# Kernel tuning notes

Measured on AMD Instinct MI355X. Metric: run time of the kernel, lower is better.

Reference implementation:

```python
import jax, jax.numpy as jnp
import numpy as np

B, N, D, H = 4, 2048, 64, 8

def setup_inputs() -> dict:
    key = jax.random.key(0)
    ks = jax.random.split(key, 6)
    s = 0.05
    return {
        "x":  jax.random.normal(ks[0], (B, N, D), dtype=jnp.float32),
        "Wq": jax.random.normal(ks[1], (D, D * H), dtype=jnp.float32) * s,
        "Wk": jax.random.normal(ks[2], (D, D * H), dtype=jnp.float32) * s,
        "Wv": jax.random.normal(ks[3], (D, D * H), dtype=jnp.float32) * s,
        "Wu": jax.random.normal(ks[4], (D * H, D), dtype=jnp.float32) * s,
        "bu": jnp.zeros((D,), dtype=jnp.float32),
    }

def reference(x, Wq, Wk, Wv, Wu, bu):
    b, n, d = x.shape
    h = Wq.shape[1] // d
    # projections: each head has full width d (per the original module)
    q = (x @ Wq).reshape(b, n, h, d).transpose(0, 2, 1, 3)  # [b,h,n,d]
    k = (x @ Wk).reshape(b, n, h, d).transpose(0, 2, 1, 3)
    v = (x @ Wv).reshape(b, n, h, d).transpose(0, 2, 1, 3)
    scores = jnp.einsum('bhnd,bhmd->bhnm', q, k) / jnp.sqrt(jnp.float32(d))
    w = jax.nn.softmax(scores, axis=-1)
    y = jnp.einsum('bhnm,bhmd->bhnd', w, v)          # [b,h,n,d]
    y = y.transpose(0, 2, 1, 3).reshape(b, n, h * d)  # [b,n,h*d]
    return y @ Wu + bu
```

## Files before the change

kernel.cpp:

```cpp
#include <hip/hip_runtime.h>
#include <hip/hip_bf16.h>

#define BB 4
#define NN 2048
#define DD 64
#define HH 8
#define DHH 512

typedef __bf16 bf16_t;
typedef __bf16 bf16x8 __attribute__((ext_vector_type(8)));
typedef __bf16 bf16x4 __attribute__((ext_vector_type(4)));
typedef float f32x4 __attribute__((ext_vector_type(4)));
typedef long long i64;
typedef i64 i64x2 __attribute__((ext_vector_type(2)));
typedef _Float16 f16_t;
typedef _Float16 f16x4 __attribute__((ext_vector_type(4)));
typedef __fp16 h16x2 __attribute__((ext_vector_type(2)));

__device__ __forceinline__ void dma16(const void* g, void* l) {
    __builtin_amdgcn_global_load_lds(
        (const __attribute__((address_space(1))) unsigned int*)g,
        (__attribute__((address_space(3))) unsigned int*)l,
        16, 0, 0);
}

#define MFMA   __builtin_amdgcn_mfma_f32_16x16x32_bf16
#define MFMA8  __builtin_amdgcn_mfma_f32_16x16x32_fp8_fp8
#define MFMA16F __builtin_amdgcn_mfma_f32_16x16x16f16

#define QSCALE 0.18033688011112042f


__global__ __launch_bounds__(256) void prep(
    const float* __restrict__ Wq, const float* __restrict__ Wk,
    const float* __restrict__ Wv, const float* __restrict__ Wu,
    bf16_t* __restrict__ Wqt, bf16_t* __restrict__ Wkt,
    bf16_t* __restrict__ Wvt, bf16_t* __restrict__ Wut)
{
    const int bid = blockIdx.x, tid = threadIdx.x;
    if (bid < 12) {
        const int m = bid >> 2, slice = bid & 3;
        const float* src = (m == 0) ? Wq : (m == 1) ? Wk : Wv;
        bf16_t* dst = (m == 0) ? Wqt : (m == 1) ? Wkt : Wvt;
        const float scale = (m == 0) ? QSCALE : 1.0f;
        const int dc = slice * 128 + (tid >> 1);
        const int kbase = (tid & 1) * 32;
        #pragma unroll
        for (int k0 = 0; k0 < 4; ++k0) {
            bf16x8 p;
            #pragma unroll
            for (int j = 0; j < 8; ++j)
                p[j] = (bf16_t)(src[(size_t)(kbase + k0 * 8 + j) * 512 + dc] * scale);
            *(bf16x8*)(dst + dc * 64 + kbase + k0 * 8) = p;
        }
    } else {
        const int kq = (bid - 12) * 128;
        const int dc = tid >> 2, sub = (tid & 3) * 32;
        #pragma unroll
        for (int k0 = 0; k0 < 4; ++k0) {
            bf16x8 p;
            #pragma unroll
            for (int j = 0; j < 8; ++j)
                p[j] = (bf16_t)Wu[(size_t)(kq + sub + k0 * 8 + j) * 64 + dc];
            *(bf16x8*)(Wut + dc * 512 + kq + sub + k0 * 8) = p;
        }
    }
}

__global__ __launch_bounds__(256) void qkv_mfma(
    const float* __restrict__ x, const bf16_t* __restrict__ Wqt,
    const bf16_t* __restrict__ Wkt, const bf16_t* __restrict__ Wvt,
    char* __restrict__ q8, char* __restrict__ k8, f16_t* __restrict__ vt)
{
    const int n0   = blockIdx.x * 64;
    const int h    = blockIdx.y;
    const int tid  = threadIdx.x;
    const int w    = tid >> 6;
    const int lane = tid & 63;
    const int quad = lane >> 4;
    const int c    = lane & 15;
    const int cq   = c & 7;
    const int l8   = lane >> 3;
    const int lg   = (lane & 7) ^ l8;
    const int lo   = l8 * 128 + lg * 16;
    const int sw0  = ((quad    ) ^ cq) * 16;
    const int sw1  = ((quad + 4) ^ cq) * 16;
    const int w2048 = w * 2048;

    __shared__ __align__(16) float  xs[64 * 64];
    __shared__ __align__(16) bf16_t Wqs[64 * 64], Wks[64 * 64], Wvs[64 * 64];

    {
        const int rloc = lane >> 4;
        const int s    = lane & 15;
        #pragma unroll
        for (int j = 0; j < 4; ++j) {
            int chunk = w * 4 + j;
            int r7 = (chunk * 4 + rloc) & 7;
            const char* src = (const char*)(x + (size_t)(n0 + chunk * 4 + rloc) * 64)
                            + ((s & 8) | ((s & 7) ^ r7)) * 16;
            dma16(src, (char*)xs + chunk * 1024);
        }
    }
    const char* qg = (const char*)Wqt + (size_t)h * 8192;
    const char* kg = (const char*)Wkt + (size_t)h * 8192;
    const char* vg = (const char*)Wvt + (size_t)h * 8192;
    dma16(qg + w2048 + lo,        (char*)Wqs + w2048);
    dma16(qg + w2048 + 1024 + lo, (char*)Wqs + w2048 + 1024);
    dma16(kg + w2048 + lo,        (char*)Wks + w2048);
    dma16(kg + w2048 + 1024 + lo, (char*)Wks + w2048 + 1024);
    dma16(vg + w2048 + lo,        (char*)Wvs + w2048);
    dma16(vg + w2048 + 1024 + lo, (char*)Wvs + w2048 + 1024);
    __syncthreads();

    auto xfrag = [&](int row, int kk) -> bf16x8 {
        const char* rbase = (const char*)xs + row * 256;
        int g0 = kk * 8 + ((quad * 2    ) ^ cq);
        int g1 = kk * 8 + ((quad * 2 + 1) ^ cq);
        f32x4 a = *(const f32x4*)(rbase + g0 * 16);
        f32x4 b = *(const f32x4*)(rbase + g1 * 16);
        bf16x8 r;
        r[0] = (bf16_t)a[0]; r[1] = (bf16_t)a[1]; r[2] = (bf16_t)a[2]; r[3] = (bf16_t)a[3];
        r[4] = (bf16_t)b[0]; r[5] = (bf16_t)b[1]; r[6] = (bf16_t)b[2]; r[7] = (bf16_t)b[3];
        return r;
    };

    bf16x8 xf0 = xfrag(w * 16 + c, 0);
    bf16x8 xf1 = xfrag(w * 16 + c, 1);

    const int gr = n0 + w * 16 + c;
    const int bb = gr >> 11, nn = gr & 2047;
    char* qrow_g = q8 + (((size_t)bb * HH + h) * NN + nn) * 64;
    char* krow_g = k8 + (((size_t)bb * HH + h) * NN + nn) * 64;
    const int nsw = nn & 3;

    #pragma unroll
    for (int mb = 0; mb < 4; ++mb) {
        const char* aq = (const char*)Wqs + (mb * 16 + c) * 128;
        const char* ak = (const char*)Wks + (mb * 16 + c) * 128;
        f32x4 accq = (f32x4){0.f, 0.f, 0.f, 0.f};
        f32x4 acck = (f32x4){0.f, 0.f, 0.f, 0.f};
        accq = MFMA(*(const bf16x8*)(aq + sw0), xf0, accq, 0, 0, 0);
        accq = MFMA(*(const bf16x8*)(aq + sw1), xf1, accq, 0, 0, 0);
        acck = MFMA(*(const bf16x8*)(ak + sw0), xf0, acck, 0, 0, 0);
        acck = MFMA(*(const bf16x8*)(ak + sw1), xf1, acck, 0, 0, 0);
        int g2  = (mb * 2 + (quad >> 1)) & 3;
        int off = ((quad & 1) * 4) + ((mb >> 1) * 8) + ((g2 ^ nsw) * 16);
        int pq = __builtin_amdgcn_cvt_pk_fp8_f32(accq[0], accq[1], 0, false);
        pq     = __builtin_amdgcn_cvt_pk_fp8_f32(accq[2], accq[3], pq, true);
        int pk = __builtin_amdgcn_cvt_pk_fp8_f32(acck[0], acck[1], 0, false);
        pk     = __builtin_amdgcn_cvt_pk_fp8_f32(acck[2], acck[3], pk, true);
        *(int*)(qrow_g + off) = pq;
        *(int*)(krow_g + off) = pk;
    }

    const char* wvrow = (const char*)Wvs + (w * 16 + c) * 128;
    bf16x8 vf0 = *(const bf16x8*)(wvrow + sw0);
    bf16x8 vf1 = *(const bf16x8*)(wvrow + sw1);

    const int bb2 = n0 >> 11;
    f16_t* vtrow_g = vt + (((size_t)bb2 * HH + h) * DD + (w * 16 + c)) * NN + (n0 & 2047);

    #pragma unroll
    for (int nb = 0; nb < 4; ++nb) {
        f32x4 acc = (f32x4){0.f, 0.f, 0.f, 0.f};
        acc = MFMA(xfrag(nb * 16 + c, 0), vf0, acc, 0, 0, 0);
        acc = MFMA(xfrag(nb * 16 + c, 1), vf1, acc, 0, 0, 0);
        f16x4 p = { (f16_t)acc[0], (f16_t)acc[1], (f16_t)acc[2], (f16_t)acc[3] };
        *(f16x4*)(vtrow_g + nb * 16 + quad * 4) = p;
    }
}

__global__ __launch_bounds__(256, 4) void flash_attn(
    const char* __restrict__ q8, const char* __restrict__ k8,
    const f16_t* __restrict__ vt, bf16_t* __restrict__ y)
{
    const int h    = blockIdx.x;
    const int n0   = blockIdx.y * 64;
    const int b    = blockIdx.z;
    const int tid  = threadIdx.x;
    const int w    = tid >> 6;
    const int lane = tid & 63;
    const int quad = lane >> 4;
    const int c    = lane & 15;
    const int l8   = lane >> 3;
    const int lg   = (lane & 7) ^ l8;
    const int ksw  = (quad ^ (c & 3)) * 16;

    __shared__ __align__(16) char SM[24576];

    const size_t bh = (size_t)(b * HH + h);
    const char* qp = q8 + bh * (size_t)(NN * 64);
    const char* kp = k8 + bh * (size_t)(NN * 64);
    const char* vp = (const char*)(vt + bh * (size_t)(DD * NN));

    i64x2 qf[4];
    #pragma unroll
    for (int cb = 0; cb < 4; ++cb)
        qf[cb] = *(const i64x2*)(qp + (size_t)(n0 + cb * 16 + c) * 64 + ksw);

    const char* kdma = kp + w * 1024 + lane * 16;
    const char* vdma = vp + (size_t)(w * 16 + l8) * 4096 + lg * 16;
    const int kro = (w * 16 + c) * 64 + ksw;
    const int vro = c * 128 + (((w * 2 + (quad >> 1)) ^ (c & 7)) * 16) + (quad & 1) * 8;

    dma16(kdma,          SM + w * 1024);
    dma16(vdma,          SM + 8192 + w * 2048);
    dma16(vdma + 32768,  SM + 8192 + w * 2048 + 1024);

    float lsum[4] = {0.f, 0.f, 0.f, 0.f};
    f32x4 o[4][4];
    #pragma unroll
    for (int db = 0; db < 4; ++db)
        #pragma unroll
        for (int cb = 0; cb < 4; ++cb) o[db][cb] = (f32x4){0.f, 0.f, 0.f, 0.f};

    __syncthreads();

    dma16(kdma + 4096,          SM + 4096 + w * 1024);
    dma16(vdma + 128,           SM + 16384 + w * 2048);
    dma16(vdma + 128 + 32768,   SM + 16384 + w * 2048 + 1024);

    for (int kt = 0; kt < 32; ++kt) {
        const int buf = kt & 1;
        if (kt > 0) {
            __syncthreads();
            if (kt < 31) {
                const size_t adv = (size_t)(kt + 1);
                dma16(kdma + adv * 4096,         SM + (buf ^ 1) * 4096 + w * 1024);
                dma16(vdma + adv * 128,          SM + 8192 + (buf ^ 1) * 8192 + w * 2048);
                dma16(vdma + adv * 128 + 32768,  SM + 8192 + (buf ^ 1) * 8192 + w * 2048 + 1024);
            }
        }
        const char* kb = SM + buf * 4096;
        const char* vb = SM + 8192 + buf * 8192;

        i64x2 kf = *(const i64x2*)(kb + kro);
        f16x4 vf[4];
        #pragma unroll
        for (int db = 0; db < 4; ++db)
            vf[db] = *(const f16x4*)(vb + vro + db * 2048);

        #pragma unroll
        for (int cb = 0; cb < 4; ++cb) {
            f32x4 s = (f32x4){0.f, 0.f, 0.f, 0.f};
            s = MFMA8(kf.x, qf[cb].x, s, 0, 0, 0);
            s = MFMA8(kf.y, qf[cb].y, s, 0, 0, 0);
            float p0 = __builtin_amdgcn_exp2f(s[0]);
            float p1 = __builtin_amdgcn_exp2f(s[1]);
            float p2 = __builtin_amdgcn_exp2f(s[2]);
            float p3 = __builtin_amdgcn_exp2f(s[3]);
            lsum[cb] += (p0 + p1) + (p2 + p3);
            h16x2 ab = __builtin_amdgcn_cvt_pkrtz(p0, p1);
            h16x2 cd = __builtin_amdgcn_cvt_pkrtz(p2, p3);
            f16x4 pf = { (f16_t)ab[0], (f16_t)ab[1], (f16_t)cd[0], (f16_t)cd[1] };
            #pragma unroll
            for (int db = 0; db < 4; ++db)
                o[db][cb] = MFMA16F(vf[db], pf, o[db][cb], 0, 0, 0);
        }
    }

    __syncthreads();

    char*  Ob = SM;
    float* Lb = (float*)(SM + 16384);

    #pragma unroll
    for (int cb = 0; cb < 4; ++cb) {
        lsum[cb] += __shfl_xor(lsum[cb], 16, 64);
        lsum[cb] += __shfl_xor(lsum[cb], 32, 64);
    }
    if (quad == 0) {
        #pragma unroll
        for (int cb = 0; cb < 4; ++cb)
            Lb[(w * 4 + cb) * 16 + c] = lsum[cb];
    }

    #pragma unroll
    for (int ww = 0; ww < 4; ++ww) {
        if (w == ww) {
            #pragma unroll
            for (int db = 0; db < 4; ++db) {
                #pragma unroll
                for (int cb = 0; cb < 4; ++cb) {
                    char* p = Ob + (size_t)(((db * 4 + cb) * 4 + quad) * 16 + c) * 16;
                    f32x4 v = o[db][cb];
                    if (ww > 0) v += *(const f32x4*)p;
                    *(f32x4*)p = v;
                }
            }
        }
        __syncthreads();
    }

    {
        const int n_loc = tid & 63;
        const int dq    = tid >> 6;
        const int qcb   = n_loc >> 4;
        const int cc    = n_loc & 15;
        float l = Lb[(0 * 4 + qcb) * 16 + cc] + Lb[(1 * 4 + qcb) * 16 + cc]
                + Lb[(2 * 4 + qcb) * 16 + cc] + Lb[(3 * 4 + qcb) * 16 + cc];
        float inv = 1.0f / l;
        float vals[16];
        #pragma unroll
        for (int q2 = 0; q2 < 4; ++q2) {
            f32x4 v = *(const f32x4*)(Ob
                    + (size_t)(((dq * 4 + qcb) * 4 + q2) * 16 + cc) * 16);
            vals[q2 * 4 + 0] = v[0]; vals[q2 * 4 + 1] = v[1];
            vals[q2 * 4 + 2] = v[2]; vals[q2 * 4 + 3] = v[3];
        }
        bf16x8 o0, o1;
        #pragma unroll
        for (int j = 0; j < 8; ++j) {
            o0[j] = (bf16_t)(vals[j] * inv);
            o1[j] = (bf16_t)(vals[8 + j] * inv);
        }
        bf16_t* yrow = y + bh * (size_t)(NN * DD) + (size_t)(n0 + n_loc) * DD + dq * 16;
        *(bf16x8*)(yrow)     = o0;
        *(bf16x8*)(yrow + 8) = o1;
    }
}

__global__ __launch_bounds__(256) void out_proj(
    const bf16_t* __restrict__ y,
    const bf16_t* __restrict__ Wut,
    const float* __restrict__ bu, float* __restrict__ out)
{
    const int rt   = blockIdx.x >> 1;
    const int dh   = blockIdx.x & 1;
    const int row0 = rt * 32;
    const int b    = row0 >> 11;
    const int nn0  = row0 & 2047;
    const int tid  = threadIdx.x;
    const int w    = tid >> 6;
    const int lane = tid & 63;
    const int quad = lane >> 4;
    const int c    = lane & 15;
    const int cq   = c & 7;

    __shared__ __align__(16) bf16_t ys[32 * 512];

    {
        const int hsel = lane >> 3;
        const int g7   = lane & 7;
        #pragma unroll
        for (int rr = 0; rr < 8; ++rr) {
            int row = w * 8 + rr;
            const char* src = (const char*)y
                + (((size_t)b * HH + hsel) * NN + nn0 + row) * 128
                + ((g7 ^ (row & 7)) * 16);
            dma16(src, (char*)ys + row * 1024);
        }
    }
    __syncthreads();

    const int rows16 = (w >> 1) * 16;
    const int mb     = dh * 2 + (w & 1);
    const char* yrow = (const char*)ys + (rows16 + c) * 1024;

    f32x4 acc = (f32x4){0.f, 0.f, 0.f, 0.f};
    #pragma unroll
    for (int kk = 0; kk < 16; ++kk) {
        int g = kk * 4 + quad;
        bf16x8 bfrag = *(const bf16x8*)(yrow + (((g & ~7) | ((g & 7) ^ cq)) * 16));
        bf16x8 afrag = *(const bf16x8*)((const char*)Wut
                        + (size_t)(mb * 16 + c) * 1024 + kk * 64 + quad * 16);
        acc = MFMA(afrag, bfrag, acc, 0, 0, 0);
    }

    float4 bb = *(const float4*)(bu + mb * 16 + quad * 4);
    float4 res = { acc[0] + bb.x, acc[1] + bb.y, acc[2] + bb.z, acc[3] + bb.w };
    float* op = out + (size_t)(row0 + rows16 + c) * DD + mb * 16 + quad * 4;
    *(float4*)op = res;
}

extern "C" void kernel_launch(void* const* d_in, const int* in_sizes, int n_in,
                              void* d_out, int out_size, void* d_ws, size_t ws_size,
                              hipStream_t stream) {
    const float* x  = (const float*)d_in[0];
    const float* Wq = (const float*)d_in[1];
    const float* Wk = (const float*)d_in[2];
    const float* Wv = (const float*)d_in[3];
    const float* Wu = (const float*)d_in[4];
    const float* bu = (const float*)d_in[5];
    float* out = (float*)d_out;

    const size_t SEG8 = (size_t)BB * HH * NN * 64;
    const size_t SEG  = SEG8 * 2;
    char* ws = (char*)d_ws;
    char*   q8  = ws;
    char*   k8  = ws + SEG8;
    f16_t*  vt  = (f16_t*)(ws + 2 * SEG8);
    bf16_t* y   = (bf16_t*)(ws + 2 * SEG8 + SEG);
    bf16_t* Wqt = (bf16_t*)(ws + 2 * SEG8 + 2 * SEG);
    bf16_t* Wkt = (bf16_t*)(ws + 2 * SEG8 + 2 * SEG + (1 << 16));
    bf16_t* Wvt = (bf16_t*)(ws + 2 * SEG8 + 2 * SEG + 2 * (1 << 16));
    bf16_t* Wut = (bf16_t*)(ws + 2 * SEG8 + 2 * SEG + 3 * (1 << 16));

    prep<<<dim3(16), dim3(256), 0, stream>>>(Wq, Wk, Wv, Wu, Wqt, Wkt, Wvt, Wut);
    qkv_mfma<<<dim3(128, 8), dim3(256), 0, stream>>>(x, Wqt, Wkt, Wvt, q8, k8, vt);
    flash_attn<<<dim3(HH, NN / 64, BB), dim3(256), 0, stream>>>(q8, k8, vt, y);
    out_proj<<<dim3(512), dim3(256), 0, stream>>>(y, Wut, bu, out);
}
```

Before: 129.0 us.

## Fuse weight prep into QKV kernel and out-projection into flash attention tail

Removes the separate prep and out_proj launches, cutting the pipeline from four kernels to two. The QKV kernel now reads fp32 weights straight from global memory, scaling and converting them to bf16 per fragment, and a few blocks also transpose Wu. Each flash-attention block bumps an atomic counter per (batch, row tile), and the last of the eight head blocks computes the output projection for those 64 rows. This trades launch overhead and a y round trip for strided uncached weight loads in the QKV kernel and serialized tail work on one block per tile.

Result: slower. 322.4 us (+149.9%).

```diff
diff --git a/kernel.cpp b/kernel.cpp
--- a/kernel.cpp
+++ b/kernel.cpp
@@ -31,64 +31,26 @@
 #define QSCALE 0.18033688011112042f
 
 
-__global__ __launch_bounds__(256) void prep(
-    const float* __restrict__ Wq, const float* __restrict__ Wk,
-    const float* __restrict__ Wv, const float* __restrict__ Wu,
-    bf16_t* __restrict__ Wqt, bf16_t* __restrict__ Wkt,
-    bf16_t* __restrict__ Wvt, bf16_t* __restrict__ Wut)
+__global__ __launch_bounds__(256, 4) void qkv_mfma(
+    const float* __restrict__ x,  const float* __restrict__ Wq,
+    const float* __restrict__ Wk, const float* __restrict__ Wv,
+    const float* __restrict__ Wu,
+    char* __restrict__ q8, char* __restrict__ k8, f16_t* __restrict__ vt,
+    bf16_t* __restrict__ Wut, unsigned* __restrict__ cnt)
 {
-    const int bid = blockIdx.x, tid = threadIdx.x;
-    if (bid < 12) {
-        const int m = bid >> 2, slice = bid & 3;
-        const float* src = (m == 0) ? Wq : (m == 1) ? Wk : Wv;
-        bf16_t* dst = (m == 0) ? Wqt : (m == 1) ? Wkt : Wvt;
-        const float scale = (m == 0) ? QSCALE : 1.0f;
-        const int dc = slice * 128 + (tid >> 1);
-        const int kbase = (tid & 1) * 32;
-        #pragma unroll
-        for (int k0 = 0; k0 < 4; ++k0) {
-            bf16x8 p;
-            #pragma unroll
-            for (int j = 0; j < 8; ++j)
-                p[j] = (bf16_t)(src[(size_t)(kbase + k0 * 8 + j) * 512 + dc] * scale);
-            *(bf16x8*)(dst + dc * 64 + kbase + k0 * 8) = p;
-        }
-    } else {
-        const int kq = (bid - 12) * 128;
-        const int dc = tid >> 2, sub = (tid & 3) * 32;
-        #pragma unroll
-        for (int k0 = 0; k0 < 4; ++k0) {
-            bf16x8 p;
-            #pragma unroll
-            for (int j = 0; j < 8; ++j)
-                p[j] = (bf16_t)Wu[(size_t)(kq + sub + k0 * 8 + j) * 64 + dc];
-            *(bf16x8*)(Wut + dc * 512 + kq + sub + k0 * 8) = p;
-        }
-    }
-}
-
-__global__ __launch_bounds__(256) void qkv_mfma(
-    const float* __restrict__ x, const bf16_t* __restrict__ Wqt,
-    const bf16_t* __restrict__ Wkt, const bf16_t* __restrict__ Wvt,
-    char* __restrict__ q8, char* __restrict__ k8, f16_t* __restrict__ vt)
-{
-    const int n0   = blockIdx.x * 64;
+    const int bx   = blockIdx.x;
     const int h    = blockIdx.y;
+    const int n0   = bx * 64;
     const int tid  = threadIdx.x;
     const int w    = tid >> 6;
     const int lane = tid & 63;
     const int quad = lane >> 4;
     const int c    = lane & 15;
     const int cq   = c & 7;
-    const int l8   = lane >> 3;
-    const int lg   = (lane & 7) ^ l8;
-    const int lo   = l8 * 128 + lg * 16;
-    const int sw0  = ((quad    ) ^ cq) * 16;
-    const int sw1  = ((quad + 4) ^ cq) * 16;
-    const int w2048 = w * 2048;
-
-    __shared__ __align__(16) float  xs[64 * 64];
-    __shared__ __align__(16) bf16_t Wqs[64 * 64], Wks[64 * 64], Wvs[64 * 64];
+
+    __shared__ __align__(16) float xs[64 * 64];
+
+    if (h == 0 && bx == 0 && tid < 128) cnt[tid] = 0;
 
     {
         const int rloc = lane >> 4;
@@ -102,15 +64,6 @@
             dma16(src, (char*)xs + chunk * 1024);
         }
     }
-    const char* qg = (const char*)Wqt + (size_t)h * 8192;
-    const char* kg = (const char*)Wkt + (size_t)h * 8192;
-    const char* vg = (const char*)Wvt + (size_t)h * 8192;
-    dma16(qg + w2048 + lo,        (char*)Wqs + w2048);
-    dma16(qg + w2048 + 1024 + lo, (char*)Wqs + w2048 + 1024);
-    dma16(kg + w2048 + lo,        (char*)Wks + w2048);
-    dma16(kg + w2048 + 1024 + lo, (char*)Wks + w2048 + 1024);
-    dma16(vg + w2048 + lo,        (char*)Wvs + w2048);
-    dma16(vg + w2048 + 1024 + lo, (char*)Wvs + w2048 + 1024);
     __syncthreads();
 
     auto xfrag = [&](int row, int kk) -> bf16x8 {
@@ -125,6 +78,14 @@
         return r;
     };
 
+    auto wfrag = [&](const float* W, int col, int k0, float scale) -> bf16x8 {
+        const float* p = W + (size_t)k0 * 512 + col;
+        bf16x8 r;
+        #pragma unroll
+        for (int j = 0; j < 8; ++j) r[j] = (bf16_t)(p[(size_t)j * 512] * scale);
+        return r;
+    };
+
     bf16x8 xf0 = xfrag(w * 16 + c, 0);
     bf16x8 xf1 = xfrag(w * 16 + c, 1);
 
@@ -132,18 +93,22 @@
     const int bb = gr >> 11, nn = gr & 2047;
     char* qrow_g = q8 + (((size_t)bb * HH + h) * NN + nn) * 64;
     char* krow_g = k8 + (((size_t)bb * HH + h) * NN + nn) * 64;
-    const int nsw = nn & 3;
+    const int nsw  = nn & 3;
+    const int hcol = h * 64;
 
     #pragma unroll
     for (int mb = 0; mb < 4; ++mb) {
-        const char* aq = (const char*)Wqs + (mb * 16 + c) * 128;
-        const char* ak = (const char*)Wks + (mb * 16 + c) * 128;
+        const int col = hcol + mb * 16 + c;
+        bf16x8 aq0 = wfrag(Wq, col, quad * 8,      QSCALE);
+        bf16x8 aq1 = wfrag(Wq, col, 32 + quad * 8, QSCALE);
+        bf16x8 ak0 = wfrag(Wk, col, quad * 8,      1.0f);
+        bf16x8 ak1 = wfrag(Wk, col, 32 + quad * 8, 1.0f);
         f32x4 accq = (f32x4){0.f, 0.f, 0.f, 0.f};
         f32x4 acck = (f32x4){0.f, 0.f, 0.f, 0.f};
-        accq = MFMA(*(const bf16x8*)(aq + sw0), xf0, accq, 0, 0, 0);
-        accq = MFMA(*(const bf16x8*)(aq + sw1), xf1, accq, 0, 0, 0);
-        acck = MFMA(*(const bf16x8*)(ak + sw0), xf0, acck, 0, 0, 0);
-        acck = MFMA(*(const bf16x8*)(ak + sw1), xf1, acck, 0, 0, 0);
+        accq = MFMA(aq0, xf0, accq, 0, 0, 0);
+        accq = MFMA(aq1, xf1, accq, 0, 0, 0);
+        acck = MFMA(ak0, xf0, acck, 0, 0, 0);
+        acck = MFMA(ak1, xf1, acck, 0, 0, 0);
         int g2  = (mb * 2 + (quad >> 1)) & 3;
         int off = ((quad & 1) * 4) + ((mb >> 1) * 8) + ((g2 ^ nsw) * 16);
         int pq = __builtin_amdgcn_cvt_pk_fp8_f32(accq[0], accq[1], 0, false);
@@ -154,9 +119,8 @@
         *(int*)(krow_g + off) = pk;
     }
 
-    const char* wvrow = (const char*)Wvs + (w * 16 + c) * 128;
-    bf16x8 vf0 = *(const bf16x8*)(wvrow + sw0);
-    bf16x8 vf1 = *(const bf16x8*)(wvrow + sw1);
+    bf16x8 vf0 = wfrag(Wv, hcol + w * 16 + c, quad * 8,      1.0f);
+    bf16x8 vf1 = wfrag(Wv, hcol + w * 16 + c, 32 + quad * 8, 1.0f);
 
     const int bb2 = n0 >> 11;
     f16_t* vtrow_g = vt + (((size_t)bb2 * HH + h) * DD + (w * 16 + c)) * NN + (n0 & 2047);
@@ -169,11 +133,26 @@
         f16x4 p = { (f16_t)acc[0], (f16_t)acc[1], (f16_t)acc[2], (f16_t)acc[3] };
         *(f16x4*)(vtrow_g + nb * 16 + quad * 4) = p;
     }
+
+    if (h == 0 && bx >= 1 && bx <= 4) {
+        const int kq = (bx - 1) * 128;
+        const int dc = tid >> 2, sub = (tid & 3) * 32;
+        #pragma unroll
+        for (int k0 = 0; k0 < 4; ++k0) {
+            bf16x8 p;
+            #pragma unroll
+            for (int j = 0; j < 8; ++j)
+                p[j] = (bf16_t)Wu[(size_t)(kq + sub + k0 * 8 + j) * 64 + dc];
+            *(bf16x8*)(Wut + dc * 512 + kq + sub + k0 * 8) = p;
+        }
+    }
 }
 
 __global__ __launch_bounds__(256, 4) void flash_attn(
     const char* __restrict__ q8, const char* __restrict__ k8,
-    const f16_t* __restrict__ vt, bf16_t* __restrict__ y)
+    const f16_t* __restrict__ vt, bf16_t* __restrict__ y,
+    const bf16_t* __restrict__ Wut, const float* __restrict__ bu,
+    float* __restrict__ out, unsigned* __restrict__ cnt)
 {
     const int h    = blockIdx.x;
     const int n0   = blockIdx.y * 64;
@@ -188,6 +167,7 @@
     const int ksw  = (quad ^ (c & 3)) * 16;
 
     __shared__ __align__(16) char SM[24576];
+    __shared__ int winflag;
 
     const size_t bh = (size_t)(b * HH + h);
     const char* qp = q8 + bh * (size_t)(NN * 64);
@@ -275,7 +255,6 @@
         for (int cb = 0; cb < 4; ++cb)
             Lb[(w * 4 + cb) * 16 + c] = lsum[cb];
     }
-
     #pragma unroll
     for (int ww = 0; ww < 4; ++ww) {
         if (w == ww) {
@@ -319,59 +298,45 @@
         *(bf16x8*)(yrow)     = o0;
         *(bf16x8*)(yrow + 8) = o1;
     }
-}
-
-__global__ __launch_bounds__(256) void out_proj(
-    const bf16_t* __restrict__ y,
-    const bf16_t* __restrict__ Wut,
-    const float* __restrict__ bu, float* __restrict__ out)
-{
-    const int rt   = blockIdx.x >> 1;
-    const int dh   = blockIdx.x & 1;
-    const int row0 = rt * 32;
-    const int b    = row0 >> 11;
-    const int nn0  = row0 & 2047;
-    const int tid  = threadIdx.x;
-    const int w    = tid >> 6;
-    const int lane = tid & 63;
-    const int quad = lane >> 4;
-    const int c    = lane & 15;
-    const int cq   = c & 7;
-
-    __shared__ __align__(16) bf16_t ys[32 * 512];
+
+    __threadfence();
+    __syncthreads();
+    if (tid == 0) {
+        unsigned old = atomicAdd(cnt + (b * 32 + (n0 >> 6)), 1u);
+        winflag = (old == 7u) ? 1 : 0;
+    }
+    __syncthreads();
+    if (!winflag) return;
+    __threadfence();
 
     {
-        const int hsel = lane >> 3;
-        const int g7   = lane & 7;
-        #pragma unroll
-        for (int rr = 0; rr < 8; ++rr) {
-            int row = w * 8 + rr;
-            const char* src = (const char*)y
-                + (((size_t)b * HH + hsel) * NN + nn0 + row) * 128
-                + ((g7 ^ (row & 7)) * 16);
-            dma16(src, (char*)ys + row * 1024);
-        }
-    }
-    __syncthreads();
-
-    const int rows16 = (w >> 1) * 16;
-    const int mb     = dh * 2 + (w & 1);
-    const char* yrow = (const char*)ys + (rows16 + c) * 1024;
-
-    f32x4 acc = (f32x4){0.f, 0.f, 0.f, 0.f};
-    #pragma unroll
-    for (int kk = 0; kk < 16; ++kk) {
-        int g = kk * 4 + quad;
-        bf16x8 bfrag = *(const bf16x8*)(yrow + (((g & ~7) | ((g & 7) ^ cq)) * 16));
-        bf16x8 afrag = *(const bf16x8*)((const char*)Wut
-                        + (size_t)(mb * 16 + c) * 1024 + kk * 64 + quad * 16);
-        acc = MFMA(afrag, bfrag, acc, 0, 0, 0);
-    }
-
-    float4 bb = *(const float4*)(bu + mb * 16 + quad * 4);
-    float4 res = { acc[0] + bb.x, acc[1] + bb.y, acc[2] + bb.z, acc[3] + bb.w };
-    float* op = out + (size_t)(row0 + rows16 + c) * DD + mb * 16 + quad * 4;
-    *(float4*)op = res;
+        const bf16_t* yb = y + (size_t)b * (HH * NN * DD);
+        const int n = n0 + w * 16 + c;
+        f32x4 acc[4];
+        #pragma unroll
+        for (int mb = 0; mb < 4; ++mb) acc[mb] = (f32x4){0.f, 0.f, 0.f, 0.f};
+
+        #pragma unroll
+        for (int kk = 0; kk < 16; ++kk) {
+            int k = kk * 32 + quad * 8;
+            const bf16_t* yrow = yb + ((size_t)(k >> 6) * NN + n) * DD + (k & 63);
+            bf16x8 bfrag = *(const bf16x8*)yrow;
+            #pragma unroll
+            for (int mb = 0; mb < 4; ++mb) {
+                bf16x8 afrag = *(const bf16x8*)((const char*)Wut
+                                + (size_t)(mb * 16 + c) * 1024 + kk * 64 + quad * 16);
+                acc[mb] = MFMA(afrag, bfrag, acc[mb], 0, 0, 0);
+            }
+        }
+        float* op = out + ((size_t)(b * NN) + n) * DD;
+        #pragma unroll
+        for (int mb = 0; mb < 4; ++mb) {
+            float4 bv = *(const float4*)(bu + mb * 16 + quad * 4);
+            *(float4*)(op + mb * 16 + quad * 4) =
+                (float4){ acc[mb][0] + bv.x, acc[mb][1] + bv.y,
+                          acc[mb][2] + bv.z, acc[mb][3] + bv.w };
+        }
+    }
 }
 
 extern "C" void kernel_launch(void* const* d_in, const int* in_sizes, int n_in,
@@ -388,17 +353,15 @@
     const size_t SEG8 = (size_t)BB * HH * NN * 64;
     const size_t SEG  = SEG8 * 2;
     char* ws = (char*)d_ws;
-    char*   q8  = ws;
-    char*   k8  = ws + SEG8;
-    f16_t*  vt  = (f16_t*)(ws + 2 * SEG8);
-    bf16_t* y   = (bf16_t*)(ws + 2 * SEG8 + SEG);
-    bf16_t* Wqt = (bf16_t*)(ws + 2 * SEG8 + 2 * SEG);
-    bf16_t* Wkt = (bf16_t*)(ws + 2 * SEG8 + 2 * SEG + (1 << 16));
-    bf16_t* Wvt = (bf16_t*)(ws + 2 * SEG8 + 2 * SEG + 2 * (1 << 16));
-    bf16_t* Wut = (bf16_t*)(ws + 2 * SEG8 + 2 * SEG + 3 * (1 << 16));
-
-    prep<<<dim3(16), dim3(256), 0, stream>>>(Wq, Wk, Wv, Wu, Wqt, Wkt, Wvt, Wut);
-    qkv_mfma<<<dim3(128, 8), dim3(256), 0, stream>>>(x, Wqt, Wkt, Wvt, q8, k8, vt);
-    flash_attn<<<dim3(HH, NN / 64, BB), dim3(256), 0, stream>>>(q8, k8, vt, y);
-    out_proj<<<dim3(512), dim3(256), 0, stream>>>(y, Wut, bu, out);
+    char*     q8  = ws;
+    char*     k8  = ws + SEG8;
+    f16_t*    vt  = (f16_t*)(ws + 2 * SEG8);
+    bf16_t*   y   = (bf16_t*)(ws + 2 * SEG8 + SEG);
+    bf16_t*   Wut = (bf16_t*)(ws + 2 * SEG8 + 2 * SEG);
+    unsigned* cnt = (unsigned*)(ws + 2 * SEG8 + 2 * SEG + (1 << 16));
+
+    qkv_mfma<<<dim3(128, 8), dim3(256), 0, stream>>>(x, Wq, Wk, Wv, Wu,
+                                                     q8, k8, vt, Wut, cnt);
+    flash_attn<<<dim3(HH, NN / 64, BB), dim3(256), 0, stream>>>(q8, k8, vt, y,
+                                                                Wut, bu, out, cnt);
 }
```
